# Performance work log

Hardware: AMD Instinct MI355X
Metric: run time of the kernel (lower is better)

Reference implementation:

```python
import jax, jax.numpy as jnp
import numpy as np


def setup_inputs() -> dict:
    key = jax.random.key(0)
    k1, k2, k3, k4, k5 = jax.random.split(key, 5)
    B, d, T = 32, 512, 2048
    return {
        "G": jax.random.normal(k1, (B, 4 * d, T), dtype=jnp.float32),
        "m1_tensor": jax.random.normal(k2, (B, d, T), dtype=jnp.float32),
        "m2_tensor": jax.random.normal(k3, (B, d, T), dtype=jnp.float32),
        "wp1": jax.random.normal(k4, (1, 5 * d), dtype=jnp.float32),
        "wp2": jax.random.normal(k5, (1, 5 * d), dtype=jnp.float32),
    }


def reference(G, m1_tensor, m2_tensor, wp1, wp2):
    # Original: per-example concat([G, m], axis=0) -> [5d, T], then per-position
    # dot(wp, column) loop -> [T]. Equivalent single contraction over feature dim.
    GM1 = jnp.concatenate([G, m1_tensor], axis=1)  # [B, 5d, T]
    GM2 = jnp.concatenate([G, m2_tensor], axis=1)  # [B, 5d, T]
    p1 = jnp.einsum("f,bft->bt", wp1[0], GM1)      # [B, T]
    p2 = jnp.einsum("f,bft->bt", wp2[0], GM2)      # [B, T]
    p1_pred = jax.nn.softmax(p1, axis=-1)
    p2_pred = jax.nn.softmax(p2, axis=-1)
    return jnp.stack([p1_pred, p2_pred], axis=1)   # [B, 2, T]
```

## Files before the change

kernel.cpp:

```cpp
#include <hip/hip_runtime.h>

#define BB    32
#define DD    512
#define FOURD 2048
#define FIVED 2560
#define TT    2048

__global__ __launch_bounds__(256) void logits_kernel(
    const float* __restrict__ G,
    const float* __restrict__ m1,
    const float* __restrict__ m2,
    const float* __restrict__ wp1,
    const float* __restrict__ wp2,
    float* __restrict__ out)
{
    __shared__ float s_wp1[FIVED];
    __shared__ float s_wp2[FIVED];
    __shared__ float4 red1[8][32];
    __shared__ float4 red2[8][32];

    const int tid    = threadIdx.x;
    const int b      = blockIdx.y;
    const int t_base = blockIdx.x * 128;

    for (int i = tid; i < FIVED; i += 256) {
        s_wp1[i] = wp1[i];
        s_wp2[i] = wp2[i];
    }
    __syncthreads();

    const int t_group = tid & 31;
    const int f_part  = tid >> 5;
    const int TV      = TT / 4;
    const int tv      = (t_base >> 2) + t_group;

    const float4* Gv  = (const float4*)(G  + (size_t)b * FOURD * TT);
    const float4* m1v = (const float4*)(m1 + (size_t)b * DD    * TT);
    const float4* m2v = (const float4*)(m2 + (size_t)b * DD    * TT);

    float4 acc1 = make_float4(0.f, 0.f, 0.f, 0.f);
    float4 acc2 = make_float4(0.f, 0.f, 0.f, 0.f);

    const int fg0 = f_part * (FOURD / 8);
    #pragma unroll 4
    for (int i = 0; i < FOURD / 8; ++i) {
        const int f = fg0 + i;
        const float4 g = Gv[(size_t)f * TV + tv];
        const float w1 = s_wp1[f];
        const float w2 = s_wp2[f];
        acc1.x += w1 * g.x; acc1.y += w1 * g.y; acc1.z += w1 * g.z; acc1.w += w1 * g.w;
        acc2.x += w2 * g.x; acc2.y += w2 * g.y; acc2.z += w2 * g.z; acc2.w += w2 * g.w;
    }

    const int fm0 = f_part * (DD / 8);
    #pragma unroll 4
    for (int i = 0; i < DD / 8; ++i) {
        const int f = fm0 + i;
        const float4 a = m1v[(size_t)f * TV + tv];
        const float4 c = m2v[(size_t)f * TV + tv];
        const float w1 = s_wp1[FOURD + f];
        const float w2 = s_wp2[FOURD + f];
        acc1.x += w1 * a.x; acc1.y += w1 * a.y; acc1.z += w1 * a.z; acc1.w += w1 * a.w;
        acc2.x += w2 * c.x; acc2.y += w2 * c.y; acc2.z += w2 * c.z; acc2.w += w2 * c.w;
    }

    red1[f_part][t_group] = acc1;
    red2[f_part][t_group] = acc2;
    __syncthreads();

    if (tid < 64) {
        const int which = tid >> 5;
        const int tg    = tid & 31;
        float4 s = make_float4(0.f, 0.f, 0.f, 0.f);
        if (which == 0) {
            #pragma unroll
            for (int p = 0; p < 8; ++p) {
                const float4 v = red1[p][tg];
                s.x += v.x; s.y += v.y; s.z += v.z; s.w += v.w;
            }
        } else {
            #pragma unroll
            for (int p = 0; p < 8; ++p) {
                const float4 v = red2[p][tg];
                s.x += v.x; s.y += v.y; s.z += v.z; s.w += v.w;
            }
        }
        float4* o = (float4*)(out + (size_t)b * 2 * TT + (size_t)which * TT + t_base);
        o[tg] = s;
    }
}

__global__ __launch_bounds__(256) void softmax_kernel(float* __restrict__ out)
{
    const int row = blockIdx.x;
    float* p = out + (size_t)row * TT;
    const int tid = threadIdx.x;

    float v[8];
    float mx = -INFINITY;
    #pragma unroll
    for (int i = 0; i < 8; ++i) {
        v[i] = p[tid + i * 256];
        mx = fmaxf(mx, v[i]);
    }

    #pragma unroll
    for (int off = 32; off > 0; off >>= 1)
        mx = fmaxf(mx, __shfl_xor(mx, off, 64));

    __shared__ float sred[4];
    const int wave = tid >> 6;
    if ((tid & 63) == 0) sred[wave] = mx;
    __syncthreads();
    if (tid == 0) {
        sred[0] = fmaxf(fmaxf(sred[0], sred[1]), fmaxf(sred[2], sred[3]));
    }
    __syncthreads();
    mx = sred[0];
    __syncthreads();

    float sum = 0.f;
    #pragma unroll
    for (int i = 0; i < 8; ++i) {
        v[i] = __expf(v[i] - mx);
        sum += v[i];
    }
    #pragma unroll
    for (int off = 32; off > 0; off >>= 1)
        sum += __shfl_xor(sum, off, 64);
    if ((tid & 63) == 0) sred[wave] = sum;
    __syncthreads();
    if (tid == 0) {
        sred[0] = sred[0] + sred[1] + sred[2] + sred[3];
    }
    __syncthreads();
    const float inv = 1.0f / sred[0];

    #pragma unroll
    for (int i = 0; i < 8; ++i)
        p[tid + i * 256] = v[i] * inv;
}

extern "C" void kernel_launch(void* const* d_in, const int* in_sizes, int n_in,
                              void* d_out, int out_size, void* d_ws, size_t ws_size,
                              hipStream_t stream) {
    const float* G   = (const float*)d_in[0];
    const float* m1  = (const float*)d_in[1];
    const float* m2  = (const float*)d_in[2];
    const float* wp1 = (const float*)d_in[3];
    const float* wp2 = (const float*)d_in[4];
    float* out = (float*)d_out;

    dim3 grid1(TT / 128, BB);
    logits_kernel<<<grid1, 256, 0, stream>>>(G, m1, m2, wp1, wp2, out);
    softmax_kernel<<<BB * 2, 256, 0, stream>>>(out);
}
```

Measured before the change: 812.3 us.

## Split feature reduction across blocks with workspace partials, fuse reduction into softmax

The logits kernel now splits the 2560-row feature contraction into 10 chunks across a third grid dimension, with each block covering 256 time positions instead of 128. Partial sums go to a workspace buffer, and the softmax kernel sums the 10 partials before the softmax. The aim is more blocks in flight and more memory-level parallelism for this bandwidth-bound contraction. The cost is extra workspace traffic and dependence on ws_size being large enough.

```diff
diff --git a/kernel.cpp b/kernel.cpp
--- a/kernel.cpp
+++ b/kernel.cpp
@@ -1,107 +1,110 @@
 #include <hip/hip_runtime.h>
 
-#define BB    32
-#define DD    512
-#define FOURD 2048
-#define FIVED 2560
-#define TT    2048
+#define BB     32
+#define DD     512
+#define FOURD  2048
+#define FIVED  2560
+#define TT     2048
+#define TV     (TT / 4)
+#define FSPLIT 10
+#define ROWS   256
 
-__global__ __launch_bounds__(256) void logits_kernel(
+__global__ __launch_bounds__(256, 4) void partial_kernel(
     const float* __restrict__ G,
     const float* __restrict__ m1,
     const float* __restrict__ m2,
     const float* __restrict__ wp1,
     const float* __restrict__ wp2,
-    float* __restrict__ out)
+    float* __restrict__ ws)
 {
-    __shared__ float s_wp1[FIVED];
-    __shared__ float s_wp2[FIVED];
-    __shared__ float4 red1[8][32];
-    __shared__ float4 red2[8][32];
+    __shared__ float s_w1[ROWS];
+    __shared__ float s_w2[ROWS];
+    __shared__ float4 red1[4][64];
+    __shared__ float4 red2[4][64];
 
-    const int tid    = threadIdx.x;
-    const int b      = blockIdx.y;
-    const int t_base = blockIdx.x * 128;
+    const int tid   = threadIdx.x;
+    const int tc    = blockIdx.x;
+    const int ys    = blockIdx.y;
+    const int b     = blockIdx.z;
+    const int fbase = ys * ROWS;
 
-    for (int i = tid; i < FIVED; i += 256) {
-        s_wp1[i] = wp1[i];
-        s_wp2[i] = wp2[i];
+    if (tid < ROWS) {
+        s_w1[tid] = wp1[fbase + tid];
+        s_w2[tid] = wp2[fbase + tid];
     }
     __syncthreads();
 
-    const int t_group = tid & 31;
-    const int f_part  = tid >> 5;
-    const int TV      = TT / 4;
-    const int tv      = (t_base >> 2) + t_group;
-
-    const float4* Gv  = (const float4*)(G  + (size_t)b * FOURD * TT);
-    const float4* m1v = (const float4*)(m1 + (size_t)b * DD    * TT);
-    const float4* m2v = (const float4*)(m2 + (size_t)b * DD    * TT);
+    const int tg = tid & 63;
+    const int fp = tid >> 6;
+    const int tv = tc * 64 + tg;
 
     float4 acc1 = make_float4(0.f, 0.f, 0.f, 0.f);
     float4 acc2 = make_float4(0.f, 0.f, 0.f, 0.f);
 
-    const int fg0 = f_part * (FOURD / 8);
-    #pragma unroll 4
-    for (int i = 0; i < FOURD / 8; ++i) {
-        const int f = fg0 + i;
-        const float4 g = Gv[(size_t)f * TV + tv];
-        const float w1 = s_wp1[f];
-        const float w2 = s_wp2[f];
-        acc1.x += w1 * g.x; acc1.y += w1 * g.y; acc1.z += w1 * g.z; acc1.w += w1 * g.w;
-        acc2.x += w2 * g.x; acc2.y += w2 * g.y; acc2.z += w2 * g.z; acc2.w += w2 * g.w;
+    if (ys < 8) {
+        const float4* Gv = (const float4*)(G + (size_t)b * FOURD * TT);
+        const int r0 = fbase + fp * 64;
+        #pragma unroll 8
+        for (int i = 0; i < 64; ++i) {
+            const float4 g = Gv[(size_t)(r0 + i) * TV + tv];
+            const float w1 = s_w1[fp * 64 + i];
+            const float w2 = s_w2[fp * 64 + i];
+            acc1.x += w1 * g.x; acc1.y += w1 * g.y; acc1.z += w1 * g.z; acc1.w += w1 * g.w;
+            acc2.x += w2 * g.x; acc2.y += w2 * g.y; acc2.z += w2 * g.z; acc2.w += w2 * g.w;
+        }
+    } else {
+        const float4* m1v = (const float4*)(m1 + (size_t)b * DD * TT);
+        const float4* m2v = (const float4*)(m2 + (size_t)b * DD * TT);
+        const int r0 = (fbase - FOURD) + fp * 64;
+        #pragma unroll 4
+        for (int i = 0; i < 64; ++i) {
+            const float4 a = m1v[(size_t)(r0 + i) * TV + tv];
+            const float4 c = m2v[(size_t)(r0 + i) * TV + tv];
+            const float w1 = s_w1[fp * 64 + i];
+            const float w2 = s_w2[fp * 64 + i];
+            acc1.x += w1 * a.x; acc1.y += w1 * a.y; acc1.z += w1 * a.z; acc1.w += w1 * a.w;
+            acc2.x += w2 * c.x; acc2.y += w2 * c.y; acc2.z += w2 * c.z; acc2.w += w2 * c.w;
+        }
     }
 
-    const int fm0 = f_part * (DD / 8);
-    #pragma unroll 4
-    for (int i = 0; i < DD / 8; ++i) {
-        const int f = fm0 + i;
-        const float4 a = m1v[(size_t)f * TV + tv];
-        const float4 c = m2v[(size_t)f * TV + tv];
-        const float w1 = s_wp1[FOURD + f];
-        const float w2 = s_wp2[FOURD + f];
-        acc1.x += w1 * a.x; acc1.y += w1 * a.y; acc1.z += w1 * a.z; acc1.w += w1 * a.w;
-        acc2.x += w2 * c.x; acc2.y += w2 * c.y; acc2.z += w2 * c.z; acc2.w += w2 * c.w;
-    }
-
-    red1[f_part][t_group] = acc1;
-    red2[f_part][t_group] = acc2;
+    red1[fp][tg] = acc1;
+    red2[fp][tg] = acc2;
     __syncthreads();
 
-    if (tid < 64) {
-        const int which = tid >> 5;
-        const int tg    = tid & 31;
+    if (tid < 128) {
+        const int which = tid >> 6;
+        const int g     = tid & 63;
         float4 s = make_float4(0.f, 0.f, 0.f, 0.f);
-        if (which == 0) {
-            #pragma unroll
-            for (int p = 0; p < 8; ++p) {
-                const float4 v = red1[p][tg];
-                s.x += v.x; s.y += v.y; s.z += v.z; s.w += v.w;
-            }
-        } else {
-            #pragma unroll
-            for (int p = 0; p < 8; ++p) {
-                const float4 v = red2[p][tg];
-                s.x += v.x; s.y += v.y; s.z += v.z; s.w += v.w;
-            }
+        #pragma unroll
+        for (int p = 0; p < 4; ++p) {
+            const float4 v = which ? red2[p][g] : red1[p][g];
+            s.x += v.x; s.y += v.y; s.z += v.z; s.w += v.w;
         }
-        float4* o = (float4*)(out + (size_t)b * 2 * TT + (size_t)which * TT + t_base);
-        o[tg] = s;
+        float4* o = (float4*)ws
+                  + ((size_t)b * 2 * FSPLIT + (size_t)which * FSPLIT + ys) * TV
+                  + tc * 64 + g;
+        *o = s;
     }
 }
 
-__global__ __launch_bounds__(256) void softmax_kernel(float* __restrict__ out)
+__global__ __launch_bounds__(256) void reduce_softmax_kernel(
+    const float* __restrict__ ws, float* __restrict__ out)
 {
-    const int row = blockIdx.x;
-    float* p = out + (size_t)row * TT;
-    const int tid = threadIdx.x;
+    const int b     = blockIdx.x >> 1;
+    const int which = blockIdx.x & 1;
+    const int tid   = threadIdx.x;
+    const float* base = ws + ((size_t)b * 2 * FSPLIT + (size_t)which * FSPLIT) * TT;
 
     float v[8];
     float mx = -INFINITY;
     #pragma unroll
     for (int i = 0; i < 8; ++i) {
-        v[i] = p[tid + i * 256];
-        mx = fmaxf(mx, v[i]);
+        const int t = tid + i * 256;
+        float s = 0.f;
+        #pragma unroll
+        for (int p = 0; p < FSPLIT; ++p) s += base[(size_t)p * TT + t];
+        v[i] = s;
+        mx = fmaxf(mx, s);
     }
 
     #pragma unroll
@@ -112,9 +115,8 @@
     const int wave = tid >> 6;
     if ((tid & 63) == 0) sred[wave] = mx;
     __syncthreads();
-    if (tid == 0) {
+    if (tid == 0)
         sred[0] = fmaxf(fmaxf(sred[0], sred[1]), fmaxf(sred[2], sred[3]));
-    }
     __syncthreads();
     mx = sred[0];
     __syncthreads();
@@ -130,12 +132,12 @@
         sum += __shfl_xor(sum, off, 64);
     if ((tid & 63) == 0) sred[wave] = sum;
     __syncthreads();
-    if (tid == 0) {
+    if (tid == 0)
         sred[0] = sred[0] + sred[1] + sred[2] + sred[3];
-    }
     __syncthreads();
     const float inv = 1.0f / sred[0];
 
+    float* p = out + ((size_t)b * 2 + which) * TT;
     #pragma unroll
     for (int i = 0; i < 8; ++i)
         p[tid + i * 256] = v[i] * inv;
@@ -150,8 +152,9 @@
     const float* wp1 = (const float*)d_in[3];
     const float* wp2 = (const float*)d_in[4];
     float* out = (float*)d_out;
+    float* ws  = (float*)d_ws;
 
-    dim3 grid1(TT / 128, BB);
-    logits_kernel<<<grid1, 256, 0, stream>>>(G, m1, m2, wp1, wp2, out);
-    softmax_kernel<<<BB * 2, 256, 0, stream>>>(out);
+    dim3 grid1(TT / 256, FSPLIT, BB);
+    partial_kernel<<<grid1, 256, 0, stream>>>(G, m1, m2, wp1, wp2, ws);
+    reduce_softmax_kernel<<<BB * 2, 256, 0, stream>>>(ws, out);
 }
```

New measurement: 835.1 us. 2.8% more time.
